# Kernel optimization log

Hardware: AMD Instinct MI355X
Metric: run time of the kernel (lower is better)

Reference implementation:

```python
import jax, jax.numpy as jnp
import numpy as np

ANCHORS_ALL = jnp.array([[10.,13.],[16.,30.],[33.,23.],[30.,61.],[62.,45.],
                         [59.,119.],[116.,90.],[156.,198.],[373.,326.]], dtype=jnp.float32)
INDICES = jnp.array([0, 1, 2], dtype=jnp.int32)   # anchor indices of level 0
ANCH_LVL = ANCHORS_ALL[0:3]                        # [nA, 2] anchors for this level
STRIDE = 8.0
N_CLS = 80
NA = 3


def _bce_logits(x, t):
    # elementwise binary_cross_entropy_with_logits (same formula as torch)
    return jnp.maximum(x, 0.0) - x * t + jnp.log1p(jnp.exp(-jnp.abs(x)))


def _iou_cxcywh(a, b):
    # a: [..., 4], b: [..., 4] (broadcastable), boxes as (cx, cy, w, h)
    ax1, ax2 = a[..., 0] - a[..., 2] * 0.5, a[..., 0] + a[..., 2] * 0.5
    ay1, ay2 = a[..., 1] - a[..., 3] * 0.5, a[..., 1] + a[..., 3] * 0.5
    bx1, bx2 = b[..., 0] - b[..., 2] * 0.5, b[..., 0] + b[..., 2] * 0.5
    by1, by2 = b[..., 1] - b[..., 3] * 0.5, b[..., 1] + b[..., 3] * 0.5
    iw = jnp.clip(jnp.minimum(ax2, bx2) - jnp.maximum(ax1, bx1), 0.0)
    ih = jnp.clip(jnp.minimum(ay2, by2) - jnp.maximum(ay1, by1), 0.0)
    inter = iw * ih
    union = (ax2 - ax1) * (ay2 - ay1) + (bx2 - bx1) * (by2 - by1) - inter
    return inter / (union + 1e-16)


def setup_inputs() -> dict:
    key = jax.random.key(0)
    ks = jax.random.split(key, 7)
    nB, nA, nH, nW, G = 8, 3, 160, 160, 32
    t_bbox = jax.random.normal(ks[0], (nB, nA, nH, nW, 4), jnp.float32)
    conf_logits = jax.random.normal(ks[1], (nB, nA, nH, nW, 1), jnp.float32)
    cls_logits = jax.random.normal(ks[2], (nB, nA, nH, nW, N_CLS), jnp.float32)
    cxy = jax.random.uniform(ks[3], (nB, G, 2), jnp.float32, 20.0, 1260.0)
    wh = jax.random.uniform(ks[4], (nB, G, 2), jnp.float32, 5.0, 60.0)
    gt_bboxes = jnp.concatenate([cxy, wh], axis=-1)           # cxcywh
    gt_cls = jax.random.randint(ks[5], (nB, G), 0, N_CLS, jnp.int32)
    gt_mask = jax.random.uniform(ks[6], (nB, G)) < 0.8        # padded-GT validity
    return dict(t_bbox=t_bbox, conf_logits=conf_logits, cls_logits=cls_logits,
                gt_bboxes=gt_bboxes, gt_cls=gt_cls, gt_mask=gt_mask)


def reference(t_bbox, conf_logits, cls_logits, gt_bboxes, gt_cls, gt_mask):
    nB, nA, nH, nW, _ = t_bbox.shape
    N = nA * nH * nW
    # ---- bbox decode (torch does this on a detached copy) ----
    sig = jax.nn.sigmoid(jax.lax.stop_gradient(t_bbox))
    yv, xv = jnp.meshgrid(jnp.arange(nH), jnp.arange(nW), indexing='ij')
    grid = jnp.stack([xv, yv], axis=-1).astype(jnp.float32).reshape(1, 1, nH, nW, 2)
    p_xy = (sig[..., 0:2] * 2.0 - 0.5 + grid) * STRIDE
    p_wh = (sig[..., 2:4] * 2.0) ** 2 * ANCH_LVL.reshape(1, nA, 1, 1, 2)
    p_bbox = jnp.concatenate([p_xy, p_wh], axis=-1).reshape(nB, N, 4)
    p_conf = jax.nn.sigmoid(jax.lax.stop_gradient(conf_logits))       # [nB,nA,nH,nW,1]
    p_cls = jax.nn.sigmoid(jax.lax.stop_gradient(cls_logits))
    cls_score = jnp.max(p_cls, axis=-1, keepdims=True)
    cls_idx = jnp.argmax(p_cls, axis=-1).reshape(nB, N)
    score = (p_conf * cls_score).reshape(nB, N)
    # ---- per-GT best-anchor matching (vectorized over [nB, G]) ----
    gw, gh = gt_bboxes[..., 2], gt_bboxes[..., 3]
    aw, ah = ANCHORS_ALL[:, 0], ANCHORS_ALL[:, 1]
    inter = jnp.minimum(gw[..., None], aw) * jnp.minimum(gh[..., None], ah)
    union = (gw * gh)[..., None] + aw * ah - inter
    anch_idx = jnp.argmax(inter / (union + 1e-16), axis=-1)           # [nB,G]
    matched = jnp.any(anch_idx[..., None] == INDICES, axis=-1)
    valid = gt_mask & matched
    ta = (anch_idx % NA).astype(jnp.int32)
    ti = jnp.clip((gt_bboxes[..., 0] / STRIDE).astype(jnp.int32), 0, nW - 1)
    tj = jnp.clip((gt_bboxes[..., 1] / STRIDE).astype(jnp.int32), 0, nH - 1)
    b_idx = jnp.arange(nB)[:, None]
    t_bb = t_bbox[b_idx, ta, tj, ti]       # [nB,G,4]
    t_cl = cls_logits[b_idx, ta, tj, ti]   # [nB,G,C]
    tgt_xy = ((gt_bboxes[..., 0:2] / STRIDE) % 1.0 + 0.5) / 2.0
    tgt_wh = jnp.sqrt(gt_bboxes[..., 2:4] / ANCH_LVL[ta]) / 2.0
    vm = valid.astype(t_bbox.dtype)
    loss_xy = jnp.sum(vm * jnp.sum(_bce_logits(t_bb[..., 0:2], tgt_xy), axis=-1))
    loss_wh = jnp.sum(vm * jnp.sum(_bce_logits(t_bb[..., 2:4], tgt_wh), axis=-1))
    onehot = jax.nn.one_hot(gt_cls, N_CLS, dtype=t_bbox.dtype)
    loss_cls = jnp.sum(vm * jnp.mean(_bce_logits(t_cl, onehot), axis=-1))
    # ---- objectness target: max IoU of every decoded box with the GTs ----
    ious = _iou_cxcywh(p_bbox[:, :, None, :], gt_bboxes[:, None, :, :])  # [nB,N,G]
    ious = jnp.where(gt_mask[:, None, :], ious, -1.0)
    has_gt = jnp.any(gt_mask, axis=-1)
    tconf = jnp.where(has_gt[:, None], jnp.max(ious, axis=-1), 0.0)
    tconf = tconf.reshape(nB, nA, nH, nW, 1)
    loss_conf = jnp.sum(_bce_logits(conf_logits, tconf))
    loss = (loss_xy + loss_wh + loss_conf + loss_cls) / nB
    return p_bbox, cls_idx, score, loss
```

## Files before the change

### kernel.cpp

```cpp
#include <hip/hip_runtime.h>

#define NB 8
#define NA 3
#define NH 160
#define NW 160
#define NCLS 80
#define NGT 32
#define NPB (NA * NH * NW)
#define TOTAL (NB * NPB)
#define NBLK (TOTAL / 256)
#define OFF_CLSIDX (TOTAL * 4)
#define OFF_SCORE  (TOTAL * 5)
#define OFF_LOSS   (TOTAL * 6)

#define F4_PER_ROW 20
#define LDS_ROW_F4 21

__device__ float g_acc = 0.0f;

__device__ __forceinline__ float det_sigmoid(float x) { return 1.0f / (1.0f + expf(-x)); }
__device__ __forceinline__ float det_bce(float x, float t) {
    return fmaxf(x, 0.0f) - x * t + log1pf(expf(-fabsf(x)));
}
__device__ __forceinline__ float det_aw3(int a) { return a == 0 ? 10.0f : (a == 1 ? 16.0f : 33.0f); }
__device__ __forceinline__ float det_ah3(int a) { return a == 0 ? 13.0f : (a == 1 ? 30.0f : 23.0f); }

__device__ __forceinline__ bool det_mask_is_u8(const void* p) {
    const unsigned int* w = (const unsigned int*)p;
    unsigned int acc = 0;
#pragma unroll
    for (int k = 0; k < 64; k++) acc |= (w[k] & 0xFFFFFF00u);
    return acc != 0;
}
__device__ __forceinline__ bool det_mask_at(const void* p, bool u8mode, int idx) {
    return u8mode ? (((const unsigned char*)p)[idx] != 0)
                  : (((const int*)p)[idx] != 0);
}

__device__ __forceinline__ float det_gt_loss(int tid,
        const float* __restrict__ t_bbox,
        const float* __restrict__ cls_logits,
        const float* __restrict__ gt_bboxes,
        const int* __restrict__ gt_cls,
        const void* __restrict__ gt_mask) {
    bool u8mode = det_mask_is_u8(gt_mask);
    int b = tid >> 5;
    int g = tid & 31;
    float4 gtb = ((const float4*)gt_bboxes)[b * NGT + g];
    float cx = gtb.x, cy = gtb.y, gw = gtb.z, gh = gtb.w;

    const float aw9[9] = {10.f,16.f,33.f,30.f,62.f,59.f,116.f,156.f,373.f};
    const float ah9[9] = {13.f,30.f,23.f,61.f,45.f,119.f,90.f,198.f,326.f};
    float garea = gw * gh;
    int aidx = 0;
    float best = -1.0f;
#pragma unroll
    for (int k = 0; k < 9; k++) {
        float inter = fminf(gw, aw9[k]) * fminf(gh, ah9[k]);
        float uni = garea + aw9[k] * ah9[k] - inter;
        float r = inter / (uni + 1e-16f);
        if (r > best) { best = r; aidx = k; }
    }
    bool valid = det_mask_at(gt_mask, u8mode, b * NGT + g) && (aidx < NA);
    int ta = aidx % NA;
    int ti = min(max((int)(cx * 0.125f), 0), NW - 1);
    int tj = min(max((int)(cy * 0.125f), 0), NH - 1);
    size_t cell = ((size_t)(b * NA + ta) * NH + tj) * NW + ti;

    float4 tb = ((const float4*)t_bbox)[cell];
    float fx = cx * 0.125f; fx -= floorf(fx);
    float fy = cy * 0.125f; fy -= floorf(fy);
    float tx = (fx + 0.5f) * 0.5f;
    float ty = (fy + 0.5f) * 0.5f;
    float tw = sqrtf(gw / det_aw3(ta)) * 0.5f;
    float th = sqrtf(gh / det_ah3(ta)) * 0.5f;

    float l = det_bce(tb.x, tx) + det_bce(tb.y, ty) +
              det_bce(tb.z, tw) + det_bce(tb.w, th);

    const float4* cl = (const float4*)(cls_logits + cell * NCLS);
    int tc = gt_cls[b * NGT + g];
    float lc = 0.0f;
#pragma unroll
    for (int c4 = 0; c4 < NCLS / 4; c4++) {
        float4 v = cl[c4];
        int c = c4 * 4;
        lc += det_bce(v.x, (c + 0 == tc) ? 1.0f : 0.0f);
        lc += det_bce(v.y, (c + 1 == tc) ? 1.0f : 0.0f);
        lc += det_bce(v.z, (c + 2 == tc) ? 1.0f : 0.0f);
        lc += det_bce(v.w, (c + 3 == tc) ? 1.0f : 0.0f);
    }
    l += lc * (1.0f / NCLS);
    return valid ? l : 0.0f;
}

__global__ __launch_bounds__(256) void det_all_k(
    const float* __restrict__ t_bbox,
    const float* __restrict__ conf_logits,
    const float* __restrict__ cls_logits,
    const float* __restrict__ gt_bboxes,
    const int* __restrict__ gt_cls,
    const void* __restrict__ gt_mask,
    float* __restrict__ out) {
    __shared__ float4 s_cls[4][16 * LDS_ROW_F4];
    __shared__ float4 s_box[NGT];
    __shared__ float2 s_am[NGT];
    __shared__ float s_part[4];

    int tid = threadIdx.x;
    int blockCell = blockIdx.x * 256;
    int gid = blockCell + tid;
    int b = gid / NPB;
    int r = gid % NPB;

    if (tid < NGT) {
        bool u8mode = det_mask_is_u8(gt_mask);
        float4 gtb = ((const float4*)gt_bboxes)[b * NGT + tid];
        float4 bx;
        bx.x = gtb.x - gtb.z * 0.5f;
        bx.y = gtb.y - gtb.w * 0.5f;
        bx.z = gtb.x + gtb.z * 0.5f;
        bx.w = gtb.y + gtb.w * 0.5f;
        s_box[tid] = bx;
        float2 am;
        am.x = gtb.z * gtb.w;
        am.y = det_mask_at(gt_mask, u8mode, b * NGT + tid) ? 1.0f : 0.0f;
        s_am[tid] = am;
    }
    __syncthreads();

    int a   = r / (NH * NW);
    int rem = r % (NH * NW);
    int j   = rem / NW;
    int i   = rem % NW;

    float4 tb = ((const float4*)t_bbox)[gid];
    float s0 = det_sigmoid(tb.x), s1 = det_sigmoid(tb.y);
    float s2 = det_sigmoid(tb.z), s3 = det_sigmoid(tb.w);
    float px = (s0 * 2.0f - 0.5f + (float)i) * 8.0f;
    float py = (s1 * 2.0f - 0.5f + (float)j) * 8.0f;
    float sw = s2 * 2.0f, sh = s3 * 2.0f;
    float pw = sw * sw * det_aw3(a);
    float ph = sh * sh * det_ah3(a);
    float4 pb; pb.x = px; pb.y = py; pb.z = pw; pb.w = ph;
    ((float4*)out)[gid] = pb;

    float px1 = px - pw * 0.5f, px2 = px + pw * 0.5f;
    float py1 = py - ph * 0.5f, py2 = py + ph * 0.5f;
    float parea = pw * ph;
    float maxiou = 0.0f;
#pragma unroll
    for (int g = 0; g < NGT; g++) {
        float4 bx = s_box[g];
        float2 am = s_am[g];
        float iw = fmaxf(fminf(px2, bx.z) - fmaxf(px1, bx.x), 0.0f);
        float ih = fmaxf(fminf(py2, bx.w) - fmaxf(py1, bx.y), 0.0f);
        float inter = iw * ih;
        float uni = parea + am.x - inter;
        float iou = inter / (uni + 1e-16f);
        maxiou = fmaxf(maxiou, (am.y != 0.0f) ? iou : 0.0f);
    }

    float confl = conf_logits[gid];
    float sconf = det_sigmoid(confl);
    float lconf = det_bce(confl, maxiou);

    if (blockIdx.x == 0)
        lconf += det_gt_loss(tid, t_bbox, cls_logits, gt_bboxes, gt_cls, gt_mask);

#pragma unroll
    for (int off = 32; off > 0; off >>= 1) lconf += __shfl_down(lconf, off, 64);
    int w = tid >> 6, l = tid & 63;
    if (l == 0) s_part[w] = lconf;
    __syncthreads();
    if (tid == 0)
        atomicAdd(&g_acc, s_part[0] + s_part[1] + s_part[2] + s_part[3]);

    int cl_ = l >> 2;
    int q   = l & 3;
    const float4* g4 = (const float4*)cls_logits;
    int wbase = blockCell + w * 64;

    float4 rbuf[5];
    {
        size_t f4base = (size_t)wbase * F4_PER_ROW;
#pragma unroll
        for (int k = 0; k < 5; ++k) rbuf[k] = g4[f4base + k * 64 + l];
    }

#pragma unroll
    for (int it = 0; it < 4; ++it) {
        __syncthreads();
#pragma unroll
        for (int k = 0; k < 5; ++k) {
            int f = k * 64 + l;
            int rr = f / F4_PER_ROW;
            int cc = f - rr * F4_PER_ROW;
            s_cls[w][rr * LDS_ROW_F4 + cc] = rbuf[k];
        }
        if (it < 3) {
            size_t f4n = (size_t)(wbase + (it + 1) * 16) * F4_PER_ROW;
#pragma unroll
            for (int k = 0; k < 5; ++k) rbuf[k] = g4[f4n + k * 64 + l];
        }
        __syncthreads();

        float mx = -1e30f;
        int mi = 0;
#pragma unroll
        for (int k = 0; k < 5; ++k) {
            int col = q * 5 + k;
            float4 v = s_cls[w][cl_ * LDS_ROW_F4 + col];
            int c = col * 4;
            if (v.x > mx) { mx = v.x; mi = c + 0; }
            if (v.y > mx) { mx = v.y; mi = c + 1; }
            if (v.z > mx) { mx = v.z; mi = c + 2; }
            if (v.w > mx) { mx = v.w; mi = c + 3; }
        }
#pragma unroll
        for (int s = 1; s < 4; s <<= 1) {
            float ov = __shfl_xor(mx, s, 64);
            int   oi = __shfl_xor(mi, s, 64);
            if (ov > mx || (ov == mx && oi < mi)) { mx = ov; mi = oi; }
        }
        int tileCell = wbase + it * 16;
        float sc = __shfl(sconf, it * 16 + cl_, 64);
        if (q == 0) {
            int cellg = tileCell + cl_;
            out[OFF_CLSIDX + cellg] = (float)mi;
            out[OFF_SCORE  + cellg] = sc * det_sigmoid(mx);
        }
    }
}

__global__ void det_fin_k(float* __restrict__ out) {
    out[OFF_LOSS] = g_acc * (1.0f / NB);
    g_acc = 0.0f;
}

extern "C" void kernel_launch(void* const* d_in, const int* in_sizes, int n_in,
                              void* d_out, int out_size, void* d_ws, size_t ws_size,
                              hipStream_t stream) {
    (void)in_sizes; (void)n_in; (void)out_size; (void)d_ws; (void)ws_size;
    const float* t_bbox      = (const float*)d_in[0];
    const float* conf_logits = (const float*)d_in[1];
    const float* cls_logits  = (const float*)d_in[2];
    const float* gt_bboxes   = (const float*)d_in[3];
    const int*   gt_cls      = (const int*)d_in[4];
    const void*  gt_mask     = (const void*)d_in[5];
    float* out = (float*)d_out;

    det_all_k<<<NBLK, 256, 0, stream>>>(t_bbox, conf_logits, cls_logits,
                                        gt_bboxes, gt_cls, gt_mask, out);
    det_fin_k<<<1, 1, 0, stream>>>(out);
}
```

Before: 321.8 us.

## Stream class logits straight into double-buffered LDS and overlap with IoU loop

```diff
diff --git a/kernel.cpp b/kernel.cpp
--- a/kernel.cpp
+++ b/kernel.cpp
@@ -14,7 +14,6 @@
 #define OFF_LOSS   (TOTAL * 6)
 
 #define F4_PER_ROW 20
-#define LDS_ROW_F4 21
 
 __device__ float g_acc = 0.0f;
 
@@ -94,6 +93,51 @@
     return valid ? l : 0.0f;
 }
 
+__device__ __forceinline__ void det_issue_tile(const float4* g4, float4* ldsbase,
+                                               size_t f4base, int l) {
+#pragma unroll
+    for (int k = 0; k < 5; ++k) {
+        __builtin_amdgcn_global_load_lds(
+            (const __attribute__((address_space(1))) void*)(g4 + f4base + k * 64 + l),
+            (__attribute__((address_space(3))) void*)(ldsbase + k * 64),
+            16, 0, 0);
+    }
+}
+
+__device__ __forceinline__ void det_scan_tile(const float4* tile, int cl_, int q,
+                                              int tileCell, float sconf, int it,
+                                              float* __restrict__ out) {
+    float mx = -1e30f;
+    int mi = 0;
+#pragma unroll
+    for (int k = 0; k < 5; ++k) {
+        int col = q * 5 + k;
+        float4 v = tile[cl_ * F4_PER_ROW + col];
+        int c = col * 4;
+        if (v.x > mx) { mx = v.x; mi = c + 0; }
+        if (v.y > mx) { mx = v.y; mi = c + 1; }
+        if (v.z > mx) { mx = v.z; mi = c + 2; }
+        if (v.w > mx) { mx = v.w; mi = c + 3; }
+    }
+#pragma unroll
+    for (int s = 1; s < 4; s <<= 1) {
+        float ov = __shfl_xor(mx, s, 64);
+        int   oi = __shfl_xor(mi, s, 64);
+        if (ov > mx || (ov == mx && oi < mi)) { mx = ov; mi = oi; }
+    }
+    float sc = __shfl(sconf, it * 16 + cl_, 64);
+    if (q == 0) {
+        int cellg = tileCell + cl_;
+        out[OFF_CLSIDX + cellg] = (float)mi;
+        out[OFF_SCORE  + cellg] = sc * det_sigmoid(mx);
+    }
+}
+
+#define DET_WAITVM(N) do { \
+    asm volatile("s_waitcnt vmcnt(" #N ")" ::: "memory"); \
+    __builtin_amdgcn_sched_barrier(0); \
+} while (0)
+
 __global__ __launch_bounds__(256) void det_all_k(
     const float* __restrict__ t_bbox,
     const float* __restrict__ conf_logits,
@@ -102,7 +146,7 @@
     const int* __restrict__ gt_cls,
     const void* __restrict__ gt_mask,
     float* __restrict__ out) {
-    __shared__ float4 s_cls[4][16 * LDS_ROW_F4];
+    __shared__ float4 s_cls[4][2][16 * F4_PER_ROW];
     __shared__ float4 s_box[NGT];
     __shared__ float2 s_am[NGT];
     __shared__ float s_part[4];
@@ -135,6 +179,7 @@
     int i   = rem % NW;
 
     float4 tb = ((const float4*)t_bbox)[gid];
+    float confl = conf_logits[gid];
     float s0 = det_sigmoid(tb.x), s1 = det_sigmoid(tb.y);
     float s2 = det_sigmoid(tb.z), s3 = det_sigmoid(tb.w);
     float px = (s0 * 2.0f - 0.5f + (float)i) * 8.0f;
@@ -145,6 +190,18 @@
     float4 pb; pb.x = px; pb.y = py; pb.z = pw; pb.w = ph;
     ((float4*)out)[gid] = pb;
 
+    int w = tid >> 6, l = tid & 63;
+    int cl_ = l >> 2;
+    int q   = l & 3;
+    const float4* g4 = (const float4*)cls_logits;
+    int wbase = blockCell + w * 64;
+    float4* t0 = &s_cls[w][0][0];
+    float4* t1 = &s_cls[w][1][0];
+    __builtin_amdgcn_sched_barrier(0);
+    det_issue_tile(g4, t0, (size_t)(wbase +  0) * F4_PER_ROW, l);
+    det_issue_tile(g4, t1, (size_t)(wbase + 16) * F4_PER_ROW, l);
+    __builtin_amdgcn_sched_barrier(0);
+
     float px1 = px - pw * 0.5f, px2 = px + pw * 0.5f;
     float py1 = py - ph * 0.5f, py2 = py + ph * 0.5f;
     float parea = pw * ph;
@@ -161,7 +218,6 @@
         maxiou = fmaxf(maxiou, (am.y != 0.0f) ? iou : 0.0f);
     }
 
-    float confl = conf_logits[gid];
     float sconf = det_sigmoid(confl);
     float lconf = det_bce(confl, maxiou);
 
@@ -170,67 +226,24 @@
 
 #pragma unroll
     for (int off = 32; off > 0; off >>= 1) lconf += __shfl_down(lconf, off, 64);
-    int w = tid >> 6, l = tid & 63;
     if (l == 0) s_part[w] = lconf;
+
+    DET_WAITVM(5);
+    det_scan_tile(t0, cl_, q, wbase +  0, sconf, 0, out);
+    __builtin_amdgcn_sched_barrier(0);
+    det_issue_tile(g4, t0, (size_t)(wbase + 32) * F4_PER_ROW, l);
+    DET_WAITVM(5);
+    det_scan_tile(t1, cl_, q, wbase + 16, sconf, 1, out);
+    __builtin_amdgcn_sched_barrier(0);
+    det_issue_tile(g4, t1, (size_t)(wbase + 48) * F4_PER_ROW, l);
+    DET_WAITVM(5);
+    det_scan_tile(t0, cl_, q, wbase + 32, sconf, 2, out);
+    DET_WAITVM(0);
+    det_scan_tile(t1, cl_, q, wbase + 48, sconf, 3, out);
+
     __syncthreads();
     if (tid == 0)
         atomicAdd(&g_acc, s_part[0] + s_part[1] + s_part[2] + s_part[3]);
-
-    int cl_ = l >> 2;
-    int q   = l & 3;
-    const float4* g4 = (const float4*)cls_logits;
-    int wbase = blockCell + w * 64;
-
-    float4 rbuf[5];
-    {
-        size_t f4base = (size_t)wbase * F4_PER_ROW;
-#pragma unroll
-        for (int k = 0; k < 5; ++k) rbuf[k] = g4[f4base + k * 64 + l];
-    }
-
-#pragma unroll
-    for (int it = 0; it < 4; ++it) {
-        __syncthreads();
-#pragma unroll
-        for (int k = 0; k < 5; ++k) {
-            int f = k * 64 + l;
-            int rr = f / F4_PER_ROW;
-            int cc = f - rr * F4_PER_ROW;
-            s_cls[w][rr * LDS_ROW_F4 + cc] = rbuf[k];
-        }
-        if (it < 3) {
-            size_t f4n = (size_t)(wbase + (it + 1) * 16) * F4_PER_ROW;
-#pragma unroll
-            for (int k = 0; k < 5; ++k) rbuf[k] = g4[f4n + k * 64 + l];
-        }
-        __syncthreads();
-
-        float mx = -1e30f;
-        int mi = 0;
-#pragma unroll
-        for (int k = 0; k < 5; ++k) {
-            int col = q * 5 + k;
-            float4 v = s_cls[w][cl_ * LDS_ROW_F4 + col];
-            int c = col * 4;
-            if (v.x > mx) { mx = v.x; mi = c + 0; }
-            if (v.y > mx) { mx = v.y; mi = c + 1; }
-            if (v.z > mx) { mx = v.z; mi = c + 2; }
-            if (v.w > mx) { mx = v.w; mi = c + 3; }
-        }
-#pragma unroll
-        for (int s = 1; s < 4; s <<= 1) {
-            float ov = __shfl_xor(mx, s, 64);
-            int   oi = __shfl_xor(mi, s, 64);
-            if (ov > mx || (ov == mx && oi < mi)) { mx = ov; mi = oi; }
-        }
-        int tileCell = wbase + it * 16;
-        float sc = __shfl(sconf, it * 16 + cl_, 64);
-        if (q == 0) {
-            int cellg = tileCell + cl_;
-            out[OFF_CLSIDX + cellg] = (float)mi;
-            out[OFF_SCORE  + cellg] = sc * det_sigmoid(mx);
-        }
-    }
 }
 
 __global__ void det_fin_k(float* __restrict__ out) {
```

After: 297.9 us. 7.4% less time.
